# Kernel tuning notes

Hardware: AMD Instinct MI355X
Metric: run time of the kernel (lower is better)

## Reference

```python
import jax, jax.numpy as jnp
import numpy as np

M = 2_097_152
C = 32
R = 256

# Same plane_axes buffer as the torch module (3 permutation matrices).
PLANE_AXES = jnp.array(
    [[[0, 1, 0], [1, 0, 0], [0, 0, 1]],
     [[0, 0, 1], [1, 0, 0], [0, 1, 0]],
     [[0, 1, 0], [0, 0, 1], [1, 0, 0]]], dtype=jnp.float32)


def setup_inputs() -> dict:
    key = jax.random.key(0)
    k1, k2 = jax.random.split(key)
    xyz = jax.random.uniform(k1, (M, 3), dtype=jnp.float32, minval=-1.0, maxval=1.0)
    # rand_init: triplane = randn * 0.001
    triplane = jax.random.normal(k2, (3, C, R, R), dtype=jnp.float32) * 0.001
    return {"xyz": xyz, "triplane": triplane}


def _grid_sample_bilinear(plane, coords):
    """plane: (C,H,W); coords: (M,2) normalized (x,y) in [-1,1].
    Matches torch F.grid_sample(mode='bilinear', padding_mode='zeros',
    align_corners=True). Returns (M,C)."""
    Cc, H, W = plane.shape
    ix = (coords[:, 0] + 1.0) * 0.5 * (W - 1)  # x indexes width
    iy = (coords[:, 1] + 1.0) * 0.5 * (H - 1)  # y indexes height
    x0 = jnp.floor(ix)
    y0 = jnp.floor(iy)
    x1 = x0 + 1.0
    y1 = y0 + 1.0
    wx1 = ix - x0
    wx0 = 1.0 - wx1
    wy1 = iy - y0
    wy0 = 1.0 - wy1

    def tap(xf, yf, w):
        valid = (xf >= 0) & (xf <= W - 1) & (yf >= 0) & (yf <= H - 1)
        xi = jnp.clip(xf, 0, W - 1).astype(jnp.int32)
        yi = jnp.clip(yf, 0, H - 1).astype(jnp.int32)
        v = plane[:, yi, xi]  # (C, M) gather
        return v * (w * valid.astype(w.dtype))[None, :]

    out = (tap(x0, y0, wx0 * wy0) + tap(x1, y0, wx1 * wy0)
           + tap(x0, y1, wx0 * wy1) + tap(x1, y1, wx1 * wy1))  # (C, M)
    return out.T  # (M, C)


def reference(xyz, triplane):
    # project_onto_planes: xyz @ inv(plane_axes), keep first two coords
    inv_planes = jnp.linalg.inv(PLANE_AXES)             # (3,3,3)
    proj = jnp.einsum('md,pdk->pmk', xyz, inv_planes)[..., :2]  # (3,M,2)
    feats = jax.vmap(_grid_sample_bilinear)(triplane, proj)      # (3,M,C)
    return feats.sum(axis=0)  # (M,C)
```

## Files before the change

kernel.cpp:

```cpp
#include <hip/hip_runtime.h>

#define R 256
#define C 32
#define NBIN 64
#define CAPB 40960
#define PPB 1024
#define CNTP 16

typedef float f32x4 __attribute__((ext_vector_type(4)));

__device__ __forceinline__ int bin_of(float px, float py, float pz) {
    int cx = min(max((int)((px + 1.0f) * 2.0f), 0), 3);
    int cy = min(max((int)((py + 1.0f) * 2.0f), 0), 3);
    int cz = min(max((int)((pz + 1.0f) * 2.0f), 0), 3);
    int oct = ((cz >> 1) << 2) | ((cy >> 1) << 1) | (cx >> 1);
    int sub = ((cz & 1) << 2) | ((cy & 1) << 1) | (cx & 1);
    return (oct << 3) | sub;
}

__device__ __forceinline__ void convert_body(const float* __restrict__ tri,
                                             ushort* __restrict__ tw, int bid) {
    int p = bid >> 8;
    int y = bid & (R - 1);
    int x = threadIdx.x;

    unsigned packed[C / 2];
#pragma unroll
    for (int i = 0; i < C / 2; ++i) {
        unsigned w = 0;
#pragma unroll
        for (int h = 0; h < 2; ++h) {
            float f = tri[(((p * C + (2 * i + h)) * R) + y) * R + x];
            unsigned u = __float_as_uint(f);
            unsigned r = (u + 0x7fffu + ((u >> 16) & 1u)) >> 16;
            w |= (r & 0xffffu) << (16 * h);
        }
        packed[i] = w;
    }
    uint4* dst = (uint4*)(tw + ((size_t)(p * R + y) * R + x) * C);
#pragma unroll
    for (int i = 0; i < 4; ++i) {
        dst[i] = make_uint4(packed[4 * i], packed[4 * i + 1],
                            packed[4 * i + 2], packed[4 * i + 3]);
    }
}

__global__ __launch_bounds__(256) void convert_scatter_kernel(
        const float* __restrict__ tri, ushort* __restrict__ tw,
        const float* __restrict__ xyz, unsigned* __restrict__ acnt,
        unsigned* __restrict__ ovcnt, f32x4* __restrict__ arena,
        f32x4* __restrict__ ov, int M) {
    int bid = blockIdx.x;
    if (bid < 3 * R) {
        convert_body(tri, tw, bid);
        return;
    }

    __shared__ unsigned lcnt[NBIN], lbase[NBIN], gbase[NBIN], lofs[NBIN];
    __shared__ f32x4 stag[PPB];
    __shared__ unsigned char sbin[PPB];

    int t = threadIdx.x;
    if (t < NBIN) { lcnt[t] = 0u; lofs[t] = 0u; }
    __syncthreads();

    int base = (bid - 3 * R) * PPB;
    float pxl[4], pyl[4], pzl[4];
    int   bl[4];
#pragma unroll
    for (int k = 0; k < 4; ++k) {
        int m = base + k * 256 + t;
        bl[k] = -1;
        if (m < M) {
            pxl[k] = xyz[3 * m + 0];
            pyl[k] = xyz[3 * m + 1];
            pzl[k] = xyz[3 * m + 2];
            bl[k]  = bin_of(pxl[k], pyl[k], pzl[k]);
            atomicAdd(&lcnt[bl[k]], 1u);
        }
    }
    __syncthreads();

    if (t < NBIN) {
        unsigned x   = lcnt[t];
        unsigned inc = x;
#pragma unroll
        for (int d = 1; d < NBIN; d <<= 1) {
            unsigned v = __shfl_up(inc, d);
            if (t >= d) inc += v;
        }
        lbase[t] = inc - x;
        gbase[t] = atomicAdd(&acnt[t * CNTP], x);
    }
    __syncthreads();

#pragma unroll
    for (int k = 0; k < 4; ++k) {
        if (bl[k] >= 0) {
            unsigned slot = atomicAdd(&lofs[bl[k]], 1u);
            unsigned j    = lbase[bl[k]] + slot;
            int m = base + k * 256 + t;
            f32x4 rec = {pxl[k], pyl[k], pzl[k], __int_as_float(m)};
            stag[j] = rec;
            sbin[j] = (unsigned char)bl[k];
        }
    }
    __syncthreads();

    int tot = (int)(lbase[NBIN - 1] + lcnt[NBIN - 1]);
    for (int j = t; j < tot; j += 256) {
        int b = sbin[j];
        unsigned pos = gbase[b] + ((unsigned)j - lbase[b]);
        f32x4 rec = stag[j];
        if (pos < CAPB) arena[(size_t)b * CAPB + pos] = rec;
        else            ov[atomicAdd(ovcnt, 1u)] = rec;
    }
}

__global__ __launch_bounds__(256) void convert_kernel(const float* __restrict__ tri,
                                                      ushort* __restrict__ tw) {
    convert_body(tri, tw, blockIdx.x);
}

__device__ __forceinline__ void tap_fma(uint4 v, float w, float* acc) {
    unsigned d[4] = {v.x, v.y, v.z, v.w};
#pragma unroll
    for (int k = 0; k < 4; ++k) {
        acc[2 * k]     = fmaf(w, __uint_as_float(d[k] << 16),          acc[2 * k]);
        acc[2 * k + 1] = fmaf(w, __uint_as_float(d[k] & 0xffff0000u), acc[2 * k + 1]);
    }
}

__device__ __forceinline__ void sample_point(float px, float py, float pz, int mo,
                                             const ushort* __restrict__ twc,
                                             float* __restrict__ out, int cq) {
    float uu[3] = {py, pz, py};
    float vv[3] = {px, px, pz};

    uint4 v[12];
    float wt[12];
#pragma unroll
    for (int p = 0; p < 3; ++p) {
        float ix = (uu[p] + 1.0f) * 0.5f * 255.0f;
        float iy = (vv[p] + 1.0f) * 0.5f * 255.0f;
        int   x0 = (int)ix;
        int   y0 = (int)iy;
        float wx1 = ix - (float)x0;
        float wy1 = iy - (float)y0;
        float wx0 = 1.0f - wx1;
        float wy0 = 1.0f - wy1;
        int x1 = min(x0 + 1, R - 1);
        int y1 = min(y0 + 1, R - 1);

        const ushort* pl = twc + (size_t)p * R * R * C;
        v[4 * p + 0] = *(const uint4*)(pl + (y0 * R + x0) * C);
        v[4 * p + 1] = *(const uint4*)(pl + (y0 * R + x1) * C);
        v[4 * p + 2] = *(const uint4*)(pl + (y1 * R + x0) * C);
        v[4 * p + 3] = *(const uint4*)(pl + (y1 * R + x1) * C);
        wt[4 * p + 0] = wx0 * wy0;
        wt[4 * p + 1] = wx1 * wy0;
        wt[4 * p + 2] = wx0 * wy1;
        wt[4 * p + 3] = wx1 * wy1;
    }

    float acc[8];
#pragma unroll
    for (int j = 0; j < 8; ++j) acc[j] = 0.0f;
#pragma unroll
    for (int s = 0; s < 12; ++s) tap_fma(v[s], wt[s], acc);

    f32x4* o = (f32x4*)(out + (size_t)mo * C + 8 * cq);
    f32x4 o0 = {acc[0], acc[1], acc[2], acc[3]};
    f32x4 o1 = {acc[4], acc[5], acc[6], acc[7]};
    __builtin_nontemporal_store(o0, o);
    __builtin_nontemporal_store(o1, o + 1);
}

__global__ __launch_bounds__(256) void sample_bins(const f32x4* __restrict__ arena,
                                                   const unsigned* __restrict__ acnt,
                                                   const unsigned* __restrict__ ovcnt,
                                                   const f32x4* __restrict__ ov,
                                                   const ushort* __restrict__ tw,
                                                   float* __restrict__ out) {
    int bid = blockIdx.x;
    int oct = bid & 7;
    int sub = (bid >> 3) & 7;
    int w   = bid >> 6;
    int bin = oct * 8 + sub;

    int quad = threadIdx.x >> 2;
    int cq   = threadIdx.x & 3;
    const ushort* twc = tw + 8 * cq;

    int n = min((int)acnt[bin * CNTP], CAPB);
    const f32x4* bk = arena + (size_t)bin * CAPB;

    int i = w * 64 + quad;
    if (i < n) {
        f32x4 r = __builtin_nontemporal_load(bk + i);
        while (true) {
            int inext = i + 32 * 64;
            bool more = inext < n;
            f32x4 rn;
            if (more) rn = __builtin_nontemporal_load(bk + inext);
            sample_point(r.x, r.y, r.z, __float_as_int(r.w), twc, out, cq);
            if (!more) break;
            r = rn;
            i = inext;
        }
    }

    int nov = (int)*ovcnt;
    if (nov > 0) {
        int gq = (bid * 256 + (int)threadIdx.x) >> 2;
        for (int j = gq; j < nov; j += 2048 * 64) {
            f32x4 r = ov[j];
            sample_point(r.x, r.y, r.z, __float_as_int(r.w), twc, out, cq);
        }
    }
}

__global__ __launch_bounds__(256) void sample_kernel(const float* __restrict__ xyz,
                                                     const ushort* __restrict__ tw,
                                                     float* __restrict__ out, int M) {
    int tid = blockIdx.x * 256 + threadIdx.x;
    int q   = tid >> 2;
    int cq  = tid & 3;
    int nq  = (gridDim.x * 256) >> 2;
    const ushort* twc = tw + 8 * cq;
    for (int m = q; m < M; m += nq) {
        float px = xyz[3 * m + 0], py = xyz[3 * m + 1], pz = xyz[3 * m + 2];
        sample_point(px, py, pz, m, twc, out, cq);
    }
}

extern "C" void kernel_launch(void* const* d_in, const int* in_sizes, int n_in,
                              void* d_out, int out_size, void* d_ws, size_t ws_size,
                              hipStream_t stream) {
    const float* xyz = (const float*)d_in[0];
    const float* tri = (const float*)d_in[1];
    float* out = (float*)d_out;

    int M = in_sizes[0] / 3;

    size_t tw_bytes  = (size_t)3 * R * R * C * sizeof(ushort);
    size_t cnt_off   = tw_bytes;
    size_t cnt_bytes = (size_t)NBIN * CNTP * sizeof(unsigned) + 128;
    size_t arena_off = cnt_off + ((cnt_bytes + 255) & ~(size_t)255);
    size_t ov_off    = arena_off + (size_t)NBIN * CAPB * sizeof(f32x4);
    size_t need      = ov_off + (size_t)M * sizeof(f32x4);

    ushort*   tw    = (ushort*)d_ws;
    unsigned* acnt  = (unsigned*)((char*)d_ws + cnt_off);
    unsigned* ovcnt = acnt + NBIN * CNTP;
    f32x4*    arena = (f32x4*)((char*)d_ws + arena_off);
    f32x4*    ov    = (f32x4*)((char*)d_ws + ov_off);

    if (ws_size >= need) {
        hipMemsetAsync(acnt, 0, cnt_bytes, stream);
        int sb = (M + PPB - 1) / PPB;
        convert_scatter_kernel<<<3 * R + sb, 256, 0, stream>>>(
            tri, tw, xyz, acnt, ovcnt, arena, ov, M);
        sample_bins<<<2048, 256, 0, stream>>>(arena, acnt, ovcnt, ov, tw, out);
    } else {
        convert_kernel<<<3 * R, 256, 0, stream>>>(tri, tw);
        sample_kernel<<<4096, 256, 0, stream>>>(xyz, tw, out, M);
    }
}
```

Measured before the change: 439.6 us.

## Refine spatial binning to 512 bins with in-block counting sort by sub-cell key

Increases the number of spatial bins from 64 to 512 and packs a 6-bit sub-cell key into the upper bits of the point index. Each sampling block now owns one bin, counting-sorts its points by sub-cell in shared memory, then samples them in that sorted order. The aim is tighter locality of triplane texel gathers, for better L1/L2 reuse. In exchange it adds shared-memory sort passes, cuts the grid to 512 blocks, and lowers the per-bin capacity, so more points may spill to the slower overflow path.

```diff
diff --git a/kernel.cpp b/kernel.cpp
--- a/kernel.cpp
+++ b/kernel.cpp
@@ -2,20 +2,24 @@
 
 #define R 256
 #define C 32
-#define NBIN 64
-#define CAPB 40960
+#define NBIN 512
+#define CAPB 6144
 #define PPB 1024
 #define CNTP 16
+#define SUBC 64
 
 typedef float f32x4 __attribute__((ext_vector_type(4)));
 
-__device__ __forceinline__ int bin_of(float px, float py, float pz) {
-    int cx = min(max((int)((px + 1.0f) * 2.0f), 0), 3);
-    int cy = min(max((int)((py + 1.0f) * 2.0f), 0), 3);
-    int cz = min(max((int)((pz + 1.0f) * 2.0f), 0), 3);
-    int oct = ((cz >> 1) << 2) | ((cy >> 1) << 1) | (cx >> 1);
-    int sub = ((cz & 1) << 2) | ((cy & 1) << 1) | (cx & 1);
-    return (oct << 3) | sub;
+__device__ __forceinline__ void bin_key_of(float px, float py, float pz,
+                                           int& bin, int& key) {
+    int gx = min(max((int)((px + 1.0f) * 16.0f), 0), 31);
+    int gy = min(max((int)((py + 1.0f) * 16.0f), 0), 31);
+    int gz = min(max((int)((pz + 1.0f) * 16.0f), 0), 31);
+    int bx = gx >> 2, by = gy >> 2, bz = gz >> 2;
+    int oct = ((bz >> 2) << 2) | ((by >> 2) << 1) | (bx >> 2);
+    int sub = ((bz & 3) << 4) | ((by & 3) << 2) | (bx & 3);
+    bin = (sub << 3) | oct;
+    key = ((gz & 3) << 4) | ((gy & 3) << 2) | (gx & 3);
 }
 
 __device__ __forceinline__ void convert_body(const float* __restrict__ tri,
@@ -58,15 +62,15 @@
 
     __shared__ unsigned lcnt[NBIN], lbase[NBIN], gbase[NBIN], lofs[NBIN];
     __shared__ f32x4 stag[PPB];
-    __shared__ unsigned char sbin[PPB];
+    __shared__ ushort sbin[PPB];
 
     int t = threadIdx.x;
-    if (t < NBIN) { lcnt[t] = 0u; lofs[t] = 0u; }
+    for (int c = t; c < NBIN; c += 256) { lcnt[c] = 0u; lofs[c] = 0u; }
     __syncthreads();
 
     int base = (bid - 3 * R) * PPB;
     float pxl[4], pyl[4], pzl[4];
-    int   bl[4];
+    int   bl[4], kl[4];
 #pragma unroll
     for (int k = 0; k < 4; ++k) {
         int m = base + k * 256 + t;
@@ -75,34 +79,43 @@
             pxl[k] = xyz[3 * m + 0];
             pyl[k] = xyz[3 * m + 1];
             pzl[k] = xyz[3 * m + 2];
-            bl[k]  = bin_of(pxl[k], pyl[k], pzl[k]);
+            bin_key_of(pxl[k], pyl[k], pzl[k], bl[k], kl[k]);
             atomicAdd(&lcnt[bl[k]], 1u);
         }
     }
     __syncthreads();
 
-    if (t < NBIN) {
-        unsigned x   = lcnt[t];
-        unsigned inc = x;
-#pragma unroll
-        for (int d = 1; d < NBIN; d <<= 1) {
-            unsigned v = __shfl_up(inc, d);
-            if (t >= d) inc += v;
-        }
-        lbase[t] = inc - x;
-        gbase[t] = atomicAdd(&acnt[t * CNTP], x);
+    if (t < 64) {
+        unsigned run = 0;
+        for (int c = 0; c < NBIN; c += 64) {
+            unsigned x   = lcnt[c + t];
+            unsigned inc = x;
+#pragma unroll
+            for (int d = 1; d < 64; d <<= 1) {
+                unsigned v = __shfl_up(inc, d);
+                if (t >= d) inc += v;
+            }
+            lbase[c + t] = run + inc - x;
+            run += __shfl(inc, 63);
+        }
+    }
+    __syncthreads();
+
+    for (int c = t; c < NBIN; c += 256) {
+        unsigned x = lcnt[c];
+        if (x) gbase[c] = atomicAdd(&acnt[c * CNTP], x);
     }
     __syncthreads();
 
 #pragma unroll
     for (int k = 0; k < 4; ++k) {
         if (bl[k] >= 0) {
-            unsigned slot = atomicAdd(&lofs[bl[k]], 1u);
-            unsigned j    = lbase[bl[k]] + slot;
+            unsigned j = lbase[bl[k]] + atomicAdd(&lofs[bl[k]], 1u);
             int m = base + k * 256 + t;
-            f32x4 rec = {pxl[k], pyl[k], pzl[k], __int_as_float(m)};
+            f32x4 rec = {pxl[k], pyl[k], pzl[k],
+                         __int_as_float((kl[k] << 21) | m)};
             stag[j] = rec;
-            sbin[j] = (unsigned char)bl[k];
+            sbin[j] = (ushort)bl[k];
         }
     }
     __syncthreads();
@@ -176,46 +189,70 @@
     __builtin_nontemporal_store(o1, o + 1);
 }
 
-__global__ __launch_bounds__(256) void sample_bins(const f32x4* __restrict__ arena,
-                                                   const unsigned* __restrict__ acnt,
-                                                   const unsigned* __restrict__ ovcnt,
-                                                   const f32x4* __restrict__ ov,
-                                                   const ushort* __restrict__ tw,
-                                                   float* __restrict__ out) {
-    int bid = blockIdx.x;
-    int oct = bid & 7;
-    int sub = (bid >> 3) & 7;
-    int w   = bid >> 6;
-    int bin = oct * 8 + sub;
-
-    int quad = threadIdx.x >> 2;
-    int cq   = threadIdx.x & 3;
-    const ushort* twc = tw + 8 * cq;
+__global__ __launch_bounds__(512, 4) void sample_bins(
+        const f32x4* __restrict__ arena, const unsigned* __restrict__ acnt,
+        const unsigned* __restrict__ ovcnt, const f32x4* __restrict__ ov,
+        const ushort* __restrict__ tw, float* __restrict__ out) {
+    __shared__ unsigned char skey[CAPB];
+    __shared__ ushort        sidx[CAPB];
+    __shared__ unsigned      scnt[SUBC], sbase[SUBC], sofs[SUBC];
+
+    int bin = blockIdx.x;
+    int t   = threadIdx.x;
+
+    if (t < SUBC) { scnt[t] = 0u; sofs[t] = 0u; }
+    __syncthreads();
 
     int n = min((int)acnt[bin * CNTP], CAPB);
     const f32x4* bk = arena + (size_t)bin * CAPB;
 
-    int i = w * 64 + quad;
-    if (i < n) {
-        f32x4 r = __builtin_nontemporal_load(bk + i);
-        while (true) {
-            int inext = i + 32 * 64;
-            bool more = inext < n;
-            f32x4 rn;
-            if (more) rn = __builtin_nontemporal_load(bk + inext);
-            sample_point(r.x, r.y, r.z, __float_as_int(r.w), twc, out, cq);
-            if (!more) break;
-            r = rn;
-            i = inext;
+    for (int i = t; i < n; i += 512) {
+        int bits = __float_as_int(bk[i].w);
+        int k    = (bits >> 21) & 63;
+        skey[i]  = (unsigned char)k;
+        atomicAdd(&scnt[k], 1u);
+    }
+    __syncthreads();
+
+    if (t < 64) {
+        unsigned x   = scnt[t];
+        unsigned inc = x;
+#pragma unroll
+        for (int d = 1; d < 64; d <<= 1) {
+            unsigned v = __shfl_up(inc, d);
+            if (t >= d) inc += v;
+        }
+        sbase[t] = inc - x;
+    }
+    __syncthreads();
+
+    for (int i = t; i < n; i += 512) {
+        int k = skey[i];
+        unsigned pos = sbase[k] + atomicAdd(&sofs[k], 1u);
+        sidx[pos] = (ushort)i;
+    }
+    __syncthreads();
+
+    int quad = t >> 2;
+    int cq   = t & 3;
+    const ushort* twc = tw + 8 * cq;
+
+    for (int j0 = 0; j0 < n; j0 += 128) {
+        int j = j0 + quad;
+        if (j < n) {
+            f32x4 r = bk[sidx[j]];
+            int mo = __float_as_int(r.w) & 0x1FFFFF;
+            sample_point(r.x, r.y, r.z, mo, twc, out, cq);
         }
     }
 
     int nov = (int)*ovcnt;
     if (nov > 0) {
-        int gq = (bid * 256 + (int)threadIdx.x) >> 2;
-        for (int j = gq; j < nov; j += 2048 * 64) {
+        int gq = (bin * 512 + t) >> 2;
+        for (int j = gq; j < nov; j += 512 * 128) {
             f32x4 r = ov[j];
-            sample_point(r.x, r.y, r.z, __float_as_int(r.w), twc, out, cq);
+            int mo = __float_as_int(r.w) & 0x1FFFFF;
+            sample_point(r.x, r.y, r.z, mo, twc, out, cq);
         }
     }
 }
@@ -261,7 +298,7 @@
         int sb = (M + PPB - 1) / PPB;
         convert_scatter_kernel<<<3 * R + sb, 256, 0, stream>>>(
             tri, tw, xyz, acnt, ovcnt, arena, ov, M);
-        sample_bins<<<2048, 256, 0, stream>>>(arena, acnt, ovcnt, ov, tw, out);
+        sample_bins<<<NBIN, 512, 0, stream>>>(arena, acnt, ovcnt, ov, tw, out);
     } else {
         convert_kernel<<<3 * R, 256, 0, stream>>>(tri, tw);
         sample_kernel<<<4096, 256, 0, stream>>>(xyz, tw, out, M);
```

Result: no change. 437.1 us (-0.6%).
